# Kernel tuning notes

Hardware: AMD Instinct MI355X
Metric: run time of the kernel (lower is better)

The kernel has to match this reference:

```python
import jax, jax.numpy as jnp
import numpy as np

N_HEADS = 16

def setup_inputs() -> dict:
    key = jax.random.key(0)
    ks = jax.random.split(key, 8)
    bs, t, h, dh = 32, 512, 1024, 64
    s = lambda k, shape: jax.random.normal(k, shape, dtype=jnp.float32) * 0.02
    return {
        "x": jax.random.normal(ks[0], (bs, t, h), dtype=jnp.float32),
        "Wq": s(ks[1], (h, h)),
        "bq": s(ks[2], (h,)),
        "Wk": s(ks[3], (h, h)),
        "bk": s(ks[4], (h,)),
        "Wv": s(ks[5], (h, dh)),
        "bv": s(ks[6], (dh,)),
        "Wo": s(ks[7], (dh, h)),
    }

def reference(x, Wq, bq, Wk, bk, Wv, bv, Wo):
    bs, t, h = x.shape
    dh = Wv.shape[1]
    nh = N_HEADS
    # projections (context == x; static_features=None path)
    q = (x @ Wq + bq).reshape(bs, t, nh, dh)   # [b,t,h,d]
    k = (x @ Wk + bk).reshape(bs, t, nh, dh)
    v = x @ Wv + bv                             # shared single-head V: [b,t,d]
    scale = dh ** -0.5
    # per-head scores [b,h,q,k]
    score = jnp.einsum('bqhd,bkhd->bhqk', q, k) * scale
    # causal mask (mask_future_timesteps=True): -inf above diagonal
    mask = jnp.triu(jnp.full((t, t), -jnp.inf, dtype=score.dtype), 1)
    score = score + mask
    prob = jax.nn.softmax(score, axis=-1)       # attn_dropout is identity (p=0)
    # broadcast shared V across heads
    attn_vec = jnp.einsum('bhqk,bkd->bhqd', prob, v)   # [b,h,t,d]
    m_attn_vec = jnp.mean(attn_vec, axis=1)            # head-mean pooling [b,t,d]
    out = m_attn_vec @ Wo                              # out_proj, no bias; out_dropout identity
    return out, attn_vec
```

## Files before the change

kernel.cpp:

```cpp
#include <hip/hip_runtime.h>
#include <hip/hip_bf16.h>
#include <math.h>

#define BS 32
#define TT 512
#define HH 1024
#define NH 16
#define DH 64
#define MM (BS*TT)
#define NCAT 2176

typedef __attribute__((ext_vector_type(8))) __bf16 bf16x8;
typedef __attribute__((ext_vector_type(4))) float  f32x4;

#define QSCALE 0.18033688011112042f

__device__ __forceinline__ void gld16(const void* g, void* l) {
    __builtin_amdgcn_global_load_lds(
        (const __attribute__((address_space(1))) unsigned int*)g,
        (__attribute__((address_space(3))) unsigned int*)l,
        16, 0, 0);
}

__global__ __launch_bounds__(256) void cvt_x(const float* __restrict__ x,
                                             __bf16* __restrict__ xb)
{
    const size_t i = ((size_t)blockIdx.x * 256 + threadIdx.x) * 8;
    float4 a = *(const float4*)(x + i);
    float4 b = *(const float4*)(x + i + 4);
    bf16x8 v;
    v[0] = (__bf16)a.x; v[1] = (__bf16)a.y; v[2] = (__bf16)a.z; v[3] = (__bf16)a.w;
    v[4] = (__bf16)b.x; v[5] = (__bf16)b.y; v[6] = (__bf16)b.z; v[7] = (__bf16)b.w;
    *(bf16x8*)(xb + i) = v;
}

__global__ __launch_bounds__(256) void prep_w(
    const float* __restrict__ Wq, const float* __restrict__ Wk,
    const float* __restrict__ Wv, const float* __restrict__ bq_,
    const float* __restrict__ bk_, const float* __restrict__ bv_,
    __bf16* __restrict__ Wt, float* __restrict__ bias_cat)
{
    __shared__ __align__(16) __bf16 tile[64][72];
    const int tid = threadIdx.x;
    const int n0 = blockIdx.x * 64;
    const int k0 = blockIdx.y * 64;

    const int n_l = tid & 63;
    const int k_b = tid >> 6;
    const int n   = n0 + n_l;
    #pragma unroll
    for (int j = 0; j < 16; ++j) {
        const int k_l = j * 4 + k_b;
        const int k   = k0 + k_l;
        float v;
        if (n < 1024)      v = Wq[(size_t)k * 1024 + n];
        else if (n < 2048) v = Wk[(size_t)k * 1024 + (n - 1024)];
        else if (n < 2112) v = Wv[(size_t)k * 64 + (n - 2048)];
        else               v = 0.f;
        tile[n_l][k_l] = (__bf16)v;
    }
    if (blockIdx.y == 0 && tid < 64) {
        const int nn = n0 + tid;
        bias_cat[nn] = (nn < 1024) ? bq_[nn]
                     : (nn < 2048) ? bk_[nn - 1024]
                     : (nn < 2112) ? bv_[nn - 2048] : 0.f;
    }
    __syncthreads();
    const int n_l2 = tid >> 2;
    const int k_l2 = (tid & 3) * 16;
    __bf16* dst = Wt + (size_t)(n0 + n_l2) * 1024 + k0 + k_l2;
    *(bf16x8*)dst       = *(const bf16x8*)&tile[n_l2][k_l2];
    *(bf16x8*)(dst + 8) = *(const bf16x8*)&tile[n_l2][k_l2 + 8];
}

__global__ __launch_bounds__(256) void gemm_qkv(
    const __bf16* __restrict__ A, const __bf16* __restrict__ B,
    const float* __restrict__ bias_cat,
    __bf16* __restrict__ Qo, __bf16* __restrict__ Ko,
    __bf16* __restrict__ Vt)
{
    __shared__ __align__(16) __bf16 sA[128 * 32];
    __shared__ __align__(16) __bf16 sB[128 * 32];

    const int tid  = threadIdx.x;
    const int wv   = tid >> 6;
    const int ln   = tid & 63;
    const int quad = ln >> 4;
    const int l16  = ln & 15;

    const int orig = blockIdx.y * 17 + blockIdx.x;
    const int swz  = (orig & 7) * 272 + (orig >> 3);
    const int m0 = (swz / 17) * 128;
    const int n0 = (swz % 17) * 128;

    const int rw = (wv & 1) * 64;
    const int cw = (wv >> 1) * 64;

    f32x4 acc[4][4];
    #pragma unroll
    for (int i = 0; i < 4; ++i)
        #pragma unroll
        for (int j = 0; j < 4; ++j) acc[i][j] = f32x4{0, 0, 0, 0};

    const int srow = wv * 16 + (ln >> 2);
    const int scol = (ln & 3) * 8;
    const __bf16* ga0 = A + (size_t)(m0 + srow) * 1024 + scol;
    const __bf16* gb0 = B + (size_t)(n0 + srow) * 1024 + scol;
    __bf16* la0 = sA + wv * 512;
    __bf16* lb0 = sB + wv * 512;

    for (int k0 = 0; k0 < 1024; k0 += 32) {
        gld16(ga0 + k0, la0);
        gld16(ga0 + (size_t)64 * 1024 + k0, la0 + 2048);
        gld16(gb0 + k0, lb0);
        gld16(gb0 + (size_t)64 * 1024 + k0, lb0 + 2048);
        __syncthreads();

        bf16x8 af[4], bfr[4];
        #pragma unroll
        for (int mt = 0; mt < 4; ++mt)
            af[mt] = *(const bf16x8*)&sA[(rw + mt * 16 + l16) * 32 + quad * 8];
        #pragma unroll
        for (int nt = 0; nt < 4; ++nt)
            bfr[nt] = *(const bf16x8*)&sB[(cw + nt * 16 + l16) * 32 + quad * 8];
        #pragma unroll
        for (int mt = 0; mt < 4; ++mt)
            #pragma unroll
            for (int nt = 0; nt < 4; ++nt)
                acc[mt][nt] = __builtin_amdgcn_mfma_f32_16x16x32_bf16(af[mt], bfr[nt], acc[mt][nt], 0, 0, 0);
        __syncthreads();
    }

    #pragma unroll
    for (int mt = 0; mt < 4; ++mt) {
        #pragma unroll
        for (int nt = 0; nt < 4; ++nt) {
            const int colb = n0 + cw + nt * 16 + l16;
            if (colb >= 2112) continue;
            const float bias = bias_cat[colb];
            #pragma unroll
            for (int r = 0; r < 4; ++r) {
                const int row = m0 + rw + mt * 16 + quad * 4 + r;
                const int b = row >> 9, t = row & 511;
                float v = acc[mt][nt][r] + bias;
                if (colb < 1024) {
                    const int h = colb >> 6, d = colb & 63;
                    Qo[(((size_t)(b * NH + h) * TT) + t) * DH + d] = (__bf16)(v * QSCALE);
                } else if (colb < 2048) {
                    const int c = colb - 1024;
                    const int h = c >> 6, d = c & 63;
                    Ko[(((size_t)(b * NH + h) * TT) + t) * DH + d] = (__bf16)v;
                } else {
                    const int d = colb - 2048;
                    Vt[((size_t)(b * DH + d)) * TT + t] = (__bf16)v;
                }
            }
        }
    }
}

__global__ __launch_bounds__(1024) void attn_mfma(
    const __bf16* __restrict__ Q, const __bf16* __restrict__ K,
    const __bf16* __restrict__ Vt, float* __restrict__ attn_vec,
    float* __restrict__ mav)
{
    __shared__ __align__(16) __bf16 sV[64][520];
    __shared__ float smav[64][65];

    const int wave = threadIdx.x >> 6;
    const int lane = threadIdx.x & 63;
    const int pair = blockIdx.x & 7;
    const int b    = blockIdx.x >> 3;
    const int bh   = b * NH + wave;
    const int quad = lane >> 4;
    const int l16  = lane & 15;

    {
        float* p = &smav[0][0];
        for (int i = threadIdx.x; i < 64 * 65; i += 1024) p[i] = 0.f;
    }

    const __bf16* Vb = Vt + (size_t)b * DH * TT;
    #pragma unroll
    for (int r = 0; r < 4; ++r) {
        const int row = wave + r * 16;
        gld16(Vb + (size_t)row * TT + lane * 8, &sV[row][0]);
    }

    const __bf16* Qbh = Q + (size_t)bh * TT * DH;
    const __bf16* Kbh = K + (size_t)bh * TT * DH;

    const int perm = ((l16 >> 2) << 3) + (l16 & 3);
    const __bf16* kp1 = Kbh + (size_t)perm * DH;
    const __bf16* kp2 = Kbh + (size_t)(perm + 4) * DH;

    __syncthreads();

    #pragma unroll 1
    for (int rep = 0; rep < 2; ++rep) {
        const int qt2 = rep ? (15 - pair) : pair;
        const int q0  = qt2 << 5;
        const int kend = q0 + 32;

        const bf16x8 qA_lo = *(const bf16x8*)(Qbh + (size_t)(q0 + l16) * DH + quad * 8);
        const bf16x8 qA_hi = *(const bf16x8*)(Qbh + (size_t)(q0 + l16) * DH + 32 + quad * 8);
        const bf16x8 qB_lo = *(const bf16x8*)(Qbh + (size_t)(q0 + 16 + l16) * DH + quad * 8);
        const bf16x8 qB_hi = *(const bf16x8*)(Qbh + (size_t)(q0 + 16 + l16) * DH + 32 + quad * 8);

        f32x4 OA[4] = {f32x4{0,0,0,0}, f32x4{0,0,0,0}, f32x4{0,0,0,0}, f32x4{0,0,0,0}};
        f32x4 OB[4] = {f32x4{0,0,0,0}, f32x4{0,0,0,0}, f32x4{0,0,0,0}, f32x4{0,0,0,0}};
        float lA = 0.f, lB = 0.f;

        bf16x8 c1a = *(const bf16x8*)(kp1 + quad * 8);
        bf16x8 c1b = *(const bf16x8*)(kp1 + 32 + quad * 8);
        bf16x8 c2a = *(const bf16x8*)(kp2 + quad * 8);
        bf16x8 c2b = *(const bf16x8*)(kp2 + 32 + quad * 8);
        const int kb1 = (32 < kend) ? 32 : 0;
        bf16x8 n1a = *(const bf16x8*)(kp1 + (size_t)kb1 * DH + quad * 8);
        bf16x8 n1b = *(const bf16x8*)(kp1 + (size_t)kb1 * DH + 32 + quad * 8);
        bf16x8 n2a = *(const bf16x8*)(kp2 + (size_t)kb1 * DH + quad * 8);
        bf16x8 n2b = *(const bf16x8*)(kp2 + (size_t)kb1 * DH + 32 + quad * 8);

        for (int kb0 = 0; kb0 < kend; kb0 += 32) {
            const int vcol = kb0 + quad * 8;
            bf16x8 vf0 = *(const bf16x8*)&sV[l16][vcol];
            bf16x8 vf1 = *(const bf16x8*)&sV[16 + l16][vcol];
            bf16x8 vf2 = *(const bf16x8*)&sV[32 + l16][vcol];
            bf16x8 vf3 = *(const bf16x8*)&sV[48 + l16][vcol];

            f32x4 s1A = __builtin_amdgcn_mfma_f32_16x16x32_bf16(c1a, qA_lo, f32x4{0,0,0,0}, 0, 0, 0);
            s1A       = __builtin_amdgcn_mfma_f32_16x16x32_bf16(c1b, qA_hi, s1A, 0, 0, 0);
            f32x4 s2A = __builtin_amdgcn_mfma_f32_16x16x32_bf16(c2a, qA_lo, f32x4{0,0,0,0}, 0, 0, 0);
            s2A       = __builtin_amdgcn_mfma_f32_16x16x32_bf16(c2b, qA_hi, s2A, 0, 0, 0);
            f32x4 s1B = __builtin_amdgcn_mfma_f32_16x16x32_bf16(c1a, qB_lo, f32x4{0,0,0,0}, 0, 0, 0);
            s1B       = __builtin_amdgcn_mfma_f32_16x16x32_bf16(c1b, qB_hi, s1B, 0, 0, 0);
            f32x4 s2B = __builtin_amdgcn_mfma_f32_16x16x32_bf16(c2a, qB_lo, f32x4{0,0,0,0}, 0, 0, 0);
            s2B       = __builtin_amdgcn_mfma_f32_16x16x32_bf16(c2b, qB_hi, s2B, 0, 0, 0);

            if (kb0 == q0) {
                const int qqA = q0 + l16, qqB = q0 + 16 + l16;
                #pragma unroll
                for (int r = 0; r < 4; ++r) {
                    const int key1 = kb0 + quad * 8 + r;
                    const int key2 = key1 + 4;
                    if (key1 > qqA) s1A[r] = -INFINITY;
                    if (key2 > qqA) s2A[r] = -INFINITY;
                    if (key1 > qqB) s1B[r] = -INFINITY;
                    if (key2 > qqB) s2B[r] = -INFINITY;
                }
            }

            bf16x8 pfA, pfB;
            float psA = 0.f, psB = 0.f;
            #pragma unroll
            for (int r = 0; r < 4; ++r) {
                float pa0 = exp2f(s1A[r]);
                float pa1 = exp2f(s2A[r]);
                float pb0 = exp2f(s1B[r]);
                float pb1 = exp2f(s2B[r]);
                psA += pa0 + pa1;
                psB += pb0 + pb1;
                pfA[r]     = (__bf16)pa0;
                pfA[4 + r] = (__bf16)pa1;
                pfB[r]     = (__bf16)pb0;
                pfB[4 + r] = (__bf16)pb1;
            }
            lA += psA;
            lB += psB;

            OA[0] = __builtin_amdgcn_mfma_f32_16x16x32_bf16(pfA, vf0, OA[0], 0, 0, 0);
            OB[0] = __builtin_amdgcn_mfma_f32_16x16x32_bf16(pfB, vf0, OB[0], 0, 0, 0);
            OA[1] = __builtin_amdgcn_mfma_f32_16x16x32_bf16(pfA, vf1, OA[1], 0, 0, 0);
            OB[1] = __builtin_amdgcn_mfma_f32_16x16x32_bf16(pfB, vf1, OB[1], 0, 0, 0);
            OA[2] = __builtin_amdgcn_mfma_f32_16x16x32_bf16(pfA, vf2, OA[2], 0, 0, 0);
            OB[2] = __builtin_amdgcn_mfma_f32_16x16x32_bf16(pfB, vf2, OB[2], 0, 0, 0);
            OA[3] = __builtin_amdgcn_mfma_f32_16x16x32_bf16(pfA, vf3, OA[3], 0, 0, 0);
            OB[3] = __builtin_amdgcn_mfma_f32_16x16x32_bf16(pfB, vf3, OB[3], 0, 0, 0);

            c1a = n1a; c1b = n1b; c2a = n2a; c2b = n2b;
            const int kbn = (kb0 + 64 < kend) ? kb0 + 64 : kend - 32;
            const __bf16* nk1 = kp1 + (size_t)kbn * DH;
            const __bf16* nk2 = kp2 + (size_t)kbn * DH;
            n1a = *(const bf16x8*)(nk1 + quad * 8);
            n1b = *(const bf16x8*)(nk1 + 32 + quad * 8);
            n2a = *(const bf16x8*)(nk2 + quad * 8);
            n2b = *(const bf16x8*)(nk2 + 32 + quad * 8);
        }

        lA += __shfl_xor(lA, 16);
        lA += __shfl_xor(lA, 32);
        lB += __shfl_xor(lB, 16);
        lB += __shfl_xor(lB, 32);

        #pragma unroll
        for (int r = 0; r < 4; ++r) {
            const float invA = 1.0f / __shfl(lA, quad * 4 + r);
            const float invB = 1.0f / __shfl(lB, quad * 4 + r);
            const int tA = q0 + quad * 4 + r;
            const int tB = tA + 16;
            const int ltA = rep * 32 + quad * 4 + r;
            const int ltB = ltA + 16;
            float* opA = attn_vec + ((size_t)bh * TT + tA) * DH + l16;
            float* opB = attn_vec + ((size_t)bh * TT + tB) * DH + l16;
            #pragma unroll
            for (int nt = 0; nt < 4; ++nt) {
                const float vA = OA[nt][r] * invA;
                const float vB = OB[nt][r] * invB;
                opA[nt * 16] = vA;
                opB[nt * 16] = vB;
                atomicAdd(&smav[ltA][nt * 16 + l16], vA * (1.f / 16.f));
                atomicAdd(&smav[ltB][nt * 16 + l16], vB * (1.f / 16.f));
            }
        }
    }

    __syncthreads();

    {
        const int row = threadIdx.x >> 4;
        const int d0  = (threadIdx.x & 15) * 4;
        const int t   = (row < 32) ? ((pair << 5) + row)
                                   : (((15 - pair) << 5) + (row - 32));
        float4 v;
        v.x = smav[row][d0];
        v.y = smav[row][d0 + 1];
        v.z = smav[row][d0 + 2];
        v.w = smav[row][d0 + 3];
        *(float4*)(mav + ((size_t)(b * TT + t)) * DH + d0) = v;
    }
}

__global__ __launch_bounds__(256) void gemm_out(
    const float* __restrict__ A, const float* __restrict__ B,
    float* __restrict__ C, int M, int N, int K)
{
    __shared__ __align__(16) __bf16 sA[64][32];
    __shared__ __align__(16) __bf16 sB[64][32];

    const int tid  = threadIdx.x;
    const int wave = tid >> 6;
    const int lane = tid & 63;
    const int m0 = blockIdx.y * 64;
    const int n0 = blockIdx.x * 64;

    f32x4 acc[4] = {f32x4{0,0,0,0}, f32x4{0,0,0,0}, f32x4{0,0,0,0}, f32x4{0,0,0,0}};

    const int ar = tid >> 2;
    const int ac = (tid & 3) * 8;
    const int bk = tid >> 3;
    const int bc = (tid & 7) * 8;
    const int quad = lane >> 4;
    const int l16  = lane & 15;

    for (int k0 = 0; k0 < K; k0 += 32) {
        const float* ap = A + (size_t)(m0 + ar) * K + k0 + ac;
        float4 a0 = *(const float4*)ap;
        float4 a1 = *(const float4*)(ap + 4);
        {
            bf16x8 av;
            av[0] = (__bf16)a0.x; av[1] = (__bf16)a0.y; av[2] = (__bf16)a0.z; av[3] = (__bf16)a0.w;
            av[4] = (__bf16)a1.x; av[5] = (__bf16)a1.y; av[6] = (__bf16)a1.z; av[7] = (__bf16)a1.w;
            *(bf16x8*)&sA[ar][ac] = av;
        }
        const float* bp = B + (size_t)(k0 + bk) * N + n0 + bc;
        float4 b0 = *(const float4*)bp;
        float4 b1 = *(const float4*)(bp + 4);
        sB[bc + 0][bk] = (__bf16)b0.x;
        sB[bc + 1][bk] = (__bf16)b0.y;
        sB[bc + 2][bk] = (__bf16)b0.z;
        sB[bc + 3][bk] = (__bf16)b0.w;
        sB[bc + 4][bk] = (__bf16)b1.x;
        sB[bc + 5][bk] = (__bf16)b1.y;
        sB[bc + 6][bk] = (__bf16)b1.z;
        sB[bc + 7][bk] = (__bf16)b1.w;
        __syncthreads();

        bf16x8 afrag = *(const bf16x8*)&sA[wave * 16 + l16][quad * 8];
        #pragma unroll
        for (int tn = 0; tn < 4; ++tn) {
            bf16x8 bfrag = *(const bf16x8*)&sB[tn * 16 + l16][quad * 8];
            acc[tn] = __builtin_amdgcn_mfma_f32_16x16x32_bf16(afrag, bfrag, acc[tn], 0, 0, 0);
        }
        __syncthreads();
    }

    #pragma unroll
    for (int tn = 0; tn < 4; ++tn) {
        #pragma unroll
        for (int r = 0; r < 4; ++r) {
            int row = m0 + wave * 16 + quad * 4 + r;
            int col = n0 + tn * 16 + l16;
            C[(size_t)row * N + col] = acc[tn][r];
        }
    }
}

extern "C" void kernel_launch(void* const* d_in, const int* in_sizes, int n_in,
                              void* d_out, int out_size, void* d_ws, size_t ws_size,
                              hipStream_t stream)
{
    const float* x  = (const float*)d_in[0];
    const float* Wq = (const float*)d_in[1];
    const float* bq = (const float*)d_in[2];
    const float* Wk = (const float*)d_in[3];
    const float* bk = (const float*)d_in[4];
    const float* Wv = (const float*)d_in[5];
    const float* bv = (const float*)d_in[6];
    const float* Wo = (const float*)d_in[7];

    float* out      = (float*)d_out;
    float* attn_vec = out + (size_t)MM * HH;

    char* ws = (char*)d_ws;
    __bf16* xb  = (__bf16*)ws;
    __bf16* Wt  = xb + (size_t)MM * HH;
    float* bias_cat = (float*)(Wt + (size_t)NCAT * HH);
    __bf16* Qb  = (__bf16*)(bias_cat + 2304);
    __bf16* Kb  = Qb + (size_t)MM * HH;
    __bf16* Vt  = Kb + (size_t)MM * HH;
    float*  mav = (float*)xb;

    cvt_x<<<MM * HH / (256 * 8), 256, 0, stream>>>(x, xb);
    prep_w<<<dim3(NCAT / 64, HH / 64), 256, 0, stream>>>(Wq, Wk, Wv, bq, bk, bv, Wt, bias_cat);
    gemm_qkv<<<dim3(NCAT / 128, MM / 128), 256, 0, stream>>>(xb, Wt, bias_cat, Qb, Kb, Vt);
    attn_mfma<<<BS * 8, 1024, 0, stream>>>(Qb, Kb, Vt, attn_vec, mav);
    gemm_out<<<dim3(HH / 64, MM / 64), 256, 0, stream>>>(mav, Wo, out, MM, HH, DH);
}
```

Before: 427.5 us.

## Split attention blocks per query tile with heavy-first order and XOR-swizzled V LDS

Each attention block now handles a single 32-row query tile instead of a balanced pair, doubling the grid and ordering blocks so the longest causal tiles launch first. The padded V shared-memory layout is replaced by an XOR swizzle on 16-byte chunks, and the head-mean scratch shrinks to 32 rows. The intent is better load balance and occupancy with less LDS, at the cost of losing the paired-tile balance within a block and reloading V per tile.

After: 435.0 us. Within noise of the previous version (+1.8%).

```diff
diff --git a/kernel.cpp b/kernel.cpp
--- a/kernel.cpp
+++ b/kernel.cpp
@@ -164,27 +164,32 @@
     const __bf16* __restrict__ Vt, float* __restrict__ attn_vec,
     float* __restrict__ mav)
 {
-    __shared__ __align__(16) __bf16 sV[64][520];
-    __shared__ float smav[64][65];
-
+    __shared__ __align__(16) __bf16 sV[64][512];
+    __shared__ float smav[32][64];
+
+    const int bid  = blockIdx.x;
+    const int qt2  = 15 - (bid >> 5);
+    const int b    = bid & 31;
     const int wave = threadIdx.x >> 6;
     const int lane = threadIdx.x & 63;
-    const int pair = blockIdx.x & 7;
-    const int b    = blockIdx.x >> 3;
-    const int bh   = b * NH + wave;
     const int quad = lane >> 4;
     const int l16  = lane & 15;
+    const int bh   = b * NH + wave;
+    const int q0   = qt2 << 5;
+    const int kend = q0 + 32;
 
     {
         float* p = &smav[0][0];
-        for (int i = threadIdx.x; i < 64 * 65; i += 1024) p[i] = 0.f;
+        p[threadIdx.x] = 0.f;
+        p[threadIdx.x + 1024] = 0.f;
     }
 
     const __bf16* Vb = Vt + (size_t)b * DH * TT;
+    const int svw = wave & 7;
     #pragma unroll
     for (int r = 0; r < 4; ++r) {
         const int row = wave + r * 16;
-        gld16(Vb + (size_t)row * TT + lane * 8, &sV[row][0]);
+        gld16(Vb + (size_t)row * TT + ((lane ^ svw) * 8), &sV[row][0]);
     }
 
     const __bf16* Qbh = Q + (size_t)bh * TT * DH;
@@ -194,139 +199,132 @@
     const __bf16* kp1 = Kbh + (size_t)perm * DH;
     const __bf16* kp2 = Kbh + (size_t)(perm + 4) * DH;
 
+    const bf16x8 qA_lo = *(const bf16x8*)(Qbh + (size_t)(q0 + l16) * DH + quad * 8);
+    const bf16x8 qA_hi = *(const bf16x8*)(Qbh + (size_t)(q0 + l16) * DH + 32 + quad * 8);
+    const bf16x8 qB_lo = *(const bf16x8*)(Qbh + (size_t)(q0 + 16 + l16) * DH + quad * 8);
+    const bf16x8 qB_hi = *(const bf16x8*)(Qbh + (size_t)(q0 + 16 + l16) * DH + 32 + quad * 8);
+
+    f32x4 OA[4] = {f32x4{0,0,0,0}, f32x4{0,0,0,0}, f32x4{0,0,0,0}, f32x4{0,0,0,0}};
+    f32x4 OB[4] = {f32x4{0,0,0,0}, f32x4{0,0,0,0}, f32x4{0,0,0,0}, f32x4{0,0,0,0}};
+    float lA = 0.f, lB = 0.f;
+
+    bf16x8 c1a = *(const bf16x8*)(kp1 + quad * 8);
+    bf16x8 c1b = *(const bf16x8*)(kp1 + 32 + quad * 8);
+    bf16x8 c2a = *(const bf16x8*)(kp2 + quad * 8);
+    bf16x8 c2b = *(const bf16x8*)(kp2 + 32 + quad * 8);
+    const int kb1 = (32 < kend) ? 32 : 0;
+    bf16x8 n1a = *(const bf16x8*)(kp1 + (size_t)kb1 * DH + quad * 8);
+    bf16x8 n1b = *(const bf16x8*)(kp1 + (size_t)kb1 * DH + 32 + quad * 8);
+    bf16x8 n2a = *(const bf16x8*)(kp2 + (size_t)kb1 * DH + quad * 8);
+    bf16x8 n2b = *(const bf16x8*)(kp2 + (size_t)kb1 * DH + 32 + quad * 8);
+
+    const int sx = l16 & 7;
+
     __syncthreads();
 
-    #pragma unroll 1
-    for (int rep = 0; rep < 2; ++rep) {
-        const int qt2 = rep ? (15 - pair) : pair;
-        const int q0  = qt2 << 5;
-        const int kend = q0 + 32;
-
-        const bf16x8 qA_lo = *(const bf16x8*)(Qbh + (size_t)(q0 + l16) * DH + quad * 8);
-        const bf16x8 qA_hi = *(const bf16x8*)(Qbh + (size_t)(q0 + l16) * DH + 32 + quad * 8);
-        const bf16x8 qB_lo = *(const bf16x8*)(Qbh + (size_t)(q0 + 16 + l16) * DH + quad * 8);
-        const bf16x8 qB_hi = *(const bf16x8*)(Qbh + (size_t)(q0 + 16 + l16) * DH + 32 + quad * 8);
-
-        f32x4 OA[4] = {f32x4{0,0,0,0}, f32x4{0,0,0,0}, f32x4{0,0,0,0}, f32x4{0,0,0,0}};
-        f32x4 OB[4] = {f32x4{0,0,0,0}, f32x4{0,0,0,0}, f32x4{0,0,0,0}, f32x4{0,0,0,0}};
-        float lA = 0.f, lB = 0.f;
-
-        bf16x8 c1a = *(const bf16x8*)(kp1 + quad * 8);
-        bf16x8 c1b = *(const bf16x8*)(kp1 + 32 + quad * 8);
-        bf16x8 c2a = *(const bf16x8*)(kp2 + quad * 8);
-        bf16x8 c2b = *(const bf16x8*)(kp2 + 32 + quad * 8);
-        const int kb1 = (32 < kend) ? 32 : 0;
-        bf16x8 n1a = *(const bf16x8*)(kp1 + (size_t)kb1 * DH + quad * 8);
-        bf16x8 n1b = *(const bf16x8*)(kp1 + (size_t)kb1 * DH + 32 + quad * 8);
-        bf16x8 n2a = *(const bf16x8*)(kp2 + (size_t)kb1 * DH + quad * 8);
-        bf16x8 n2b = *(const bf16x8*)(kp2 + (size_t)kb1 * DH + 32 + quad * 8);
-
-        for (int kb0 = 0; kb0 < kend; kb0 += 32) {
-            const int vcol = kb0 + quad * 8;
-            bf16x8 vf0 = *(const bf16x8*)&sV[l16][vcol];
-            bf16x8 vf1 = *(const bf16x8*)&sV[16 + l16][vcol];
-            bf16x8 vf2 = *(const bf16x8*)&sV[32 + l16][vcol];
-            bf16x8 vf3 = *(const bf16x8*)&sV[48 + l16][vcol];
-
-            f32x4 s1A = __builtin_amdgcn_mfma_f32_16x16x32_bf16(c1a, qA_lo, f32x4{0,0,0,0}, 0, 0, 0);
-            s1A       = __builtin_amdgcn_mfma_f32_16x16x32_bf16(c1b, qA_hi, s1A, 0, 0, 0);
-            f32x4 s2A = __builtin_amdgcn_mfma_f32_16x16x32_bf16(c2a, qA_lo, f32x4{0,0,0,0}, 0, 0, 0);
-            s2A       = __builtin_amdgcn_mfma_f32_16x16x32_bf16(c2b, qA_hi, s2A, 0, 0, 0);
-            f32x4 s1B = __builtin_amdgcn_mfma_f32_16x16x32_bf16(c1a, qB_lo, f32x4{0,0,0,0}, 0, 0, 0);
-            s1B       = __builtin_amdgcn_mfma_f32_16x16x32_bf16(c1b, qB_hi, s1B, 0, 0, 0);
-            f32x4 s2B = __builtin_amdgcn_mfma_f32_16x16x32_bf16(c2a, qB_lo, f32x4{0,0,0,0}, 0, 0, 0);
-            s2B       = __builtin_amdgcn_mfma_f32_16x16x32_bf16(c2b, qB_hi, s2B, 0, 0, 0);
-
-            if (kb0 == q0) {
-                const int qqA = q0 + l16, qqB = q0 + 16 + l16;
-                #pragma unroll
-                for (int r = 0; r < 4; ++r) {
-                    const int key1 = kb0 + quad * 8 + r;
-                    const int key2 = key1 + 4;
-                    if (key1 > qqA) s1A[r] = -INFINITY;
-                    if (key2 > qqA) s2A[r] = -INFINITY;
-                    if (key1 > qqB) s1B[r] = -INFINITY;
-                    if (key2 > qqB) s2B[r] = -INFINITY;
-                }
-            }
-
-            bf16x8 pfA, pfB;
-            float psA = 0.f, psB = 0.f;
+    for (int kb0 = 0; kb0 < kend; kb0 += 32) {
+        const int vg = (((kb0 >> 3) + quad) ^ sx) * 8;
+        bf16x8 vf0 = *(const bf16x8*)&sV[l16][vg];
+        bf16x8 vf1 = *(const bf16x8*)&sV[16 + l16][vg];
+        bf16x8 vf2 = *(const bf16x8*)&sV[32 + l16][vg];
+        bf16x8 vf3 = *(const bf16x8*)&sV[48 + l16][vg];
+
+        f32x4 s1A = __builtin_amdgcn_mfma_f32_16x16x32_bf16(c1a, qA_lo, f32x4{0,0,0,0}, 0, 0, 0);
+        s1A       = __builtin_amdgcn_mfma_f32_16x16x32_bf16(c1b, qA_hi, s1A, 0, 0, 0);
+        f32x4 s2A = __builtin_amdgcn_mfma_f32_16x16x32_bf16(c2a, qA_lo, f32x4{0,0,0,0}, 0, 0, 0);
+        s2A       = __builtin_amdgcn_mfma_f32_16x16x32_bf16(c2b, qA_hi, s2A, 0, 0, 0);
+        f32x4 s1B = __builtin_amdgcn_mfma_f32_16x16x32_bf16(c1a, qB_lo, f32x4{0,0,0,0}, 0, 0, 0);
+        s1B       = __builtin_amdgcn_mfma_f32_16x16x32_bf16(c1b, qB_hi, s1B, 0, 0, 0);
+        f32x4 s2B = __builtin_amdgcn_mfma_f32_16x16x32_bf16(c2a, qB_lo, f32x4{0,0,0,0}, 0, 0, 0);
+        s2B       = __builtin_amdgcn_mfma_f32_16x16x32_bf16(c2b, qB_hi, s2B, 0, 0, 0);
+
+        if (kb0 == q0) {
+            const int qqA = q0 + l16, qqB = q0 + 16 + l16;
             #pragma unroll
             for (int r = 0; r < 4; ++r) {
-                float pa0 = exp2f(s1A[r]);
-                float pa1 = exp2f(s2A[r]);
-                float pb0 = exp2f(s1B[r]);
-                float pb1 = exp2f(s2B[r]);
-                psA += pa0 + pa1;
-                psB += pb0 + pb1;
-                pfA[r]     = (__bf16)pa0;
-                pfA[4 + r] = (__bf16)pa1;
-                pfB[r]     = (__bf16)pb0;
-                pfB[4 + r] = (__bf16)pb1;
+                const int key1 = kb0 + quad * 8 + r;
+                const int key2 = key1 + 4;
+                if (key1 > qqA) s1A[r] = -INFINITY;
+                if (key2 > qqA) s2A[r] = -INFINITY;
+                if (key1 > qqB) s1B[r] = -INFINITY;
+                if (key2 > qqB) s2B[r] = -INFINITY;
             }
-            lA += psA;
-            lB += psB;
-
-            OA[0] = __builtin_amdgcn_mfma_f32_16x16x32_bf16(pfA, vf0, OA[0], 0, 0, 0);
-            OB[0] = __builtin_amdgcn_mfma_f32_16x16x32_bf16(pfB, vf0, OB[0], 0, 0, 0);
-            OA[1] = __builtin_amdgcn_mfma_f32_16x16x32_bf16(pfA, vf1, OA[1], 0, 0, 0);
-            OB[1] = __builtin_amdgcn_mfma_f32_16x16x32_bf16(pfB, vf1, OB[1], 0, 0, 0);
-            OA[2] = __builtin_amdgcn_mfma_f32_16x16x32_bf16(pfA, vf2, OA[2], 0, 0, 0);
-            OB[2] = __builtin_amdgcn_mfma_f32_16x16x32_bf16(pfB, vf2, OB[2], 0, 0, 0);
-            OA[3] = __builtin_amdgcn_mfma_f32_16x16x32_bf16(pfA, vf3, OA[3], 0, 0, 0);
-            OB[3] = __builtin_amdgcn_mfma_f32_16x16x32_bf16(pfB, vf3, OB[3], 0, 0, 0);
-
-            c1a = n1a; c1b = n1b; c2a = n2a; c2b = n2b;
-            const int kbn = (kb0 + 64 < kend) ? kb0 + 64 : kend - 32;
-            const __bf16* nk1 = kp1 + (size_t)kbn * DH;
-            const __bf16* nk2 = kp2 + (size_t)kbn * DH;
-            n1a = *(const bf16x8*)(nk1 + quad * 8);
-            n1b = *(const bf16x8*)(nk1 + 32 + quad * 8);
-            n2a = *(const bf16x8*)(nk2 + quad * 8);
-            n2b = *(const bf16x8*)(nk2 + 32 + quad * 8);
-        }
-
-        lA += __shfl_xor(lA, 16);
-        lA += __shfl_xor(lA, 32);
-        lB += __shfl_xor(lB, 16);
-        lB += __shfl_xor(lB, 32);
-
+        }
+
+        bf16x8 pfA, pfB;
+        float psA = 0.f, psB = 0.f;
         #pragma unroll
         for (int r = 0; r < 4; ++r) {
-            const float invA = 1.0f / __shfl(lA, quad * 4 + r);
-            const float invB = 1.0f / __shfl(lB, quad * 4 + r);
-            const int tA = q0 + quad * 4 + r;
-            const int tB = tA + 16;
-            const int ltA = rep * 32 + quad * 4 + r;
-            const int ltB = ltA + 16;
-            float* opA = attn_vec + ((size_t)bh * TT + tA) * DH + l16;
-            float* opB = attn_vec + ((size_t)bh * TT + tB) * DH + l16;
-            #pragma unroll
-            for (int nt = 0; nt < 4; ++nt) {
-                const float vA = OA[nt][r] * invA;
-                const float vB = OB[nt][r] * invB;
-                opA[nt * 16] = vA;
-                opB[nt * 16] = vB;
-                atomicAdd(&smav[ltA][nt * 16 + l16], vA * (1.f / 16.f));
-                atomicAdd(&smav[ltB][nt * 16 + l16], vB * (1.f / 16.f));
-            }
+            float pa0 = exp2f(s1A[r]);
+            float pa1 = exp2f(s2A[r]);
+            float pb0 = exp2f(s1B[r]);
+            float pb1 = exp2f(s2B[r]);
+            psA += pa0 + pa1;
+            psB += pb0 + pb1;
+            pfA[r]     = (__bf16)pa0;
+            pfA[4 + r] = (__bf16)pa1;
+            pfB[r]     = (__bf16)pb0;
+            pfB[4 + r] = (__bf16)pb1;
+        }
+        lA += psA;
+        lB += psB;
+
+        OA[0] = __builtin_amdgcn_mfma_f32_16x16x32_bf16(pfA, vf0, OA[0], 0, 0, 0);
+        OB[0] = __builtin_amdgcn_mfma_f32_16x16x32_bf16(pfB, vf0, OB[0], 0, 0, 0);
+        OA[1] = __builtin_amdgcn_mfma_f32_16x16x32_bf16(pfA, vf1, OA[1], 0, 0, 0);
+        OB[1] = __builtin_amdgcn_mfma_f32_16x16x32_bf16(pfB, vf1, OB[1], 0, 0, 0);
+        OA[2] = __builtin_amdgcn_mfma_f32_16x16x32_bf16(pfA, vf2, OA[2], 0, 0, 0);
+        OB[2] = __builtin_amdgcn_mfma_f32_16x16x32_bf16(pfB, vf2, OB[2], 0, 0, 0);
+        OA[3] = __builtin_amdgcn_mfma_f32_16x16x32_bf16(pfA, vf3, OA[3], 0, 0, 0);
+        OB[3] = __builtin_amdgcn_mfma_f32_16x16x32_bf16(pfB, vf3, OB[3], 0, 0, 0);
+
+        c1a = n1a; c1b = n1b; c2a = n2a; c2b = n2b;
+        const int kbn = (kb0 + 64 < kend) ? kb0 + 64 : kend - 32;
+        const __bf16* nk1 = kp1 + (size_t)kbn * DH;
+        const __bf16* nk2 = kp2 + (size_t)kbn * DH;
+        n1a = *(const bf16x8*)(nk1 + quad * 8);
+        n1b = *(const bf16x8*)(nk1 + 32 + quad * 8);
+        n2a = *(const bf16x8*)(nk2 + quad * 8);
+        n2b = *(const bf16x8*)(nk2 + 32 + quad * 8);
+    }
+
+    lA += __shfl_xor(lA, 16);
+    lA += __shfl_xor(lA, 32);
+    lB += __shfl_xor(lB, 16);
+    lB += __shfl_xor(lB, 32);
+
+    #pragma unroll
+    for (int r = 0; r < 4; ++r) {
+        const float invA = 1.0f / __shfl(lA, quad * 4 + r);
+        const float invB = 1.0f / __shfl(lB, quad * 4 + r);
+        const int ltA = quad * 4 + r;
+        const int ltB = ltA + 16;
+        const int tA = q0 + ltA;
+        const int tB = q0 + ltB;
+        float* opA = attn_vec + ((size_t)bh * TT + tA) * DH + l16;
+        float* opB = attn_vec + ((size_t)bh * TT + tB) * DH + l16;
+        #pragma unroll
+        for (int nt = 0; nt < 4; ++nt) {
+            const float vA = OA[nt][r] * invA;
+            const float vB = OB[nt][r] * invB;
+            opA[nt * 16] = vA;
+            opB[nt * 16] = vB;
+            atomicAdd(&smav[ltA][nt * 16 + l16], vA * (1.f / 16.f));
+            atomicAdd(&smav[ltB][nt * 16 + l16], vB * (1.f / 16.f));
         }
     }
 
     __syncthreads();
 
-    {
+    if (threadIdx.x < 512) {
         const int row = threadIdx.x >> 4;
         const int d0  = (threadIdx.x & 15) * 4;
-        const int t   = (row < 32) ? ((pair << 5) + row)
-                                   : (((15 - pair) << 5) + (row - 32));
         float4 v;
         v.x = smav[row][d0];
         v.y = smav[row][d0 + 1];
         v.z = smav[row][d0 + 2];
         v.w = smav[row][d0 + 3];
-        *(float4*)(mav + ((size_t)(b * TT + t)) * DH + d0) = v;
+        *(float4*)(mav + ((size_t)(b * TT + q0 + row)) * DH + d0) = v;
     }
 }
 
@@ -423,6 +421,6 @@
     cvt_x<<<MM * HH / (256 * 8), 256, 0, stream>>>(x, xb);
     prep_w<<<dim3(NCAT / 64, HH / 64), 256, 0, stream>>>(Wq, Wk, Wv, bq, bk, bv, Wt, bias_cat);
     gemm_qkv<<<dim3(NCAT / 128, MM / 128), 256, 0, stream>>>(xb, Wt, bias_cat, Qb, Kb, Vt);
-    attn_mfma<<<BS * 8, 1024, 0, stream>>>(Qb, Kb, Vt, attn_vec, mav);
+    attn_mfma<<<BS * NH, 1024, 0, stream>>>(Qb, Kb, Vt, attn_vec, mav);
     gemm_out<<<dim3(HH / 64, MM / 64), 256, 0, stream>>>(mav, Wo, out, MM, HH, DH);
 }
```
